# Optimization experiments

Hardware: AMD Instinct MI355X
Metric: run time of the kernel (lower is better)

## Reference

```python
import jax, jax.numpy as jnp
import numpy as np
import math

B, T, C_IN = 4, 2048, 1024
HIDDEN, HEADS = 1024, 8
HEAD_DIM = HIDDEN // HEADS
OUT_DIM = 1024
EPS = 1e-8


def setup_inputs() -> dict:
    key = jax.random.key(0)
    ks = jax.random.split(key, 12)
    s_in = 1.0 / math.sqrt(C_IN)
    s_h = 1.0 / math.sqrt(HIDDEN)
    x = jax.random.normal(ks[0], (B, T, C_IN), dtype=jnp.float32)
    # causal keep-mask (True = keep), broadcast over batch
    attn_mask = jnp.broadcast_to(jnp.tril(jnp.ones((T, T), dtype=bool)), (B, T, T))
    Wu = jax.random.normal(ks[1], (HIDDEN, C_IN), dtype=jnp.float32) * s_in
    bu = jnp.zeros((HIDDEN,), dtype=jnp.float32)
    Wv = jax.random.normal(ks[2], (HIDDEN, C_IN), dtype=jnp.float32) * s_in
    bv = jnp.zeros((HIDDEN,), dtype=jnp.float32)
    Wq = jax.random.normal(ks[3], (HIDDEN, C_IN), dtype=jnp.float32) * s_in
    bq = jnp.zeros((HIDDEN,), dtype=jnp.float32)
    Wk = jax.random.normal(ks[4], (HIDDEN, C_IN), dtype=jnp.float32) * s_in
    bk = jnp.zeros((HIDDEN,), dtype=jnp.float32)
    Wf = jax.random.normal(ks[5], (OUT_DIM, HIDDEN), dtype=jnp.float32) * s_h
    bf = jnp.zeros((OUT_DIM,), dtype=jnp.float32)
    g_norm = jnp.ones((HIDDEN,), dtype=jnp.float32)
    return {"x": x, "attn_mask": attn_mask, "Wu": Wu, "bu": bu, "Wv": Wv,
            "bv": bv, "Wq": Wq, "bq": bq, "Wk": Wk, "bk": bk,
            "Wf": Wf, "bf": bf, "g_norm": g_norm}


def _heads(t):  # (B,T,HIDDEN) -> (B,H,T,D)
    b, s, _ = t.shape
    return t.reshape(b, s, HEADS, HEAD_DIM).transpose(0, 2, 1, 3)


def reference(x, attn_mask, Wu, bu, Wv, bv, Wq, bq, Wk, bk, Wf, bf, g_norm):
    silu = jax.nn.silu
    U = silu(x @ Wu.T + bu)
    V = silu(x @ Wv.T + bv)
    Q = silu(x @ Wq.T + bq)
    K = silu(x @ Wk.T + bk)
    Qh, Kh, Vh = _heads(Q), _heads(K), _heads(V)
    scale = 1.0 / math.sqrt(HEAD_DIM)
    logits = jnp.einsum('bhtd,bhsd->bhts', Qh, Kh) * scale
    A = jnp.maximum(silu(logits), 0.0)
    A = jnp.where(attn_mask[:, None, :, :], A, 0.0)
    denom = A.sum(axis=-1, keepdims=True)
    A = jnp.where(denom > 1e-12, A / (denom + EPS), 0.0)
    AVh = jnp.einsum('bhts,bhsd->bhtd', A, Vh)
    AV = AVh.transpose(0, 2, 1, 3).reshape(x.shape[0], x.shape[1], HIDDEN)
    # RMSNorm (torch nn.RMSNorm default eps = dtype eps)
    rms_eps = jnp.finfo(AV.dtype).eps
    AV_norm = AV * jax.lax.rsqrt(jnp.mean(AV * AV, axis=-1, keepdims=True) + rms_eps) * g_norm
    UV = AV_norm * U
    return UV @ Wf.T + bf
```

## Files before the change

### kernel.cpp

```cpp
#include <hip/hip_runtime.h>
#include <hip/hip_bf16.h>
#include <stdint.h>

#define Tlen  2048
#define M_TOK 8192

typedef __attribute__((ext_vector_type(8))) __bf16 bf16x8;
typedef __attribute__((ext_vector_type(4))) float  f32x4;
typedef unsigned short u16;
typedef unsigned int   u32;
typedef unsigned long long u64;

__device__ __forceinline__ float b2f(u16 u) {
  union { float f; u32 i; } v; v.i = ((u32)u) << 16; return v.f;
}
__device__ __forceinline__ u16 f2b(float f) {
  u32 x = __float_as_uint(f);
  return (u16)((x + 0x7FFFu + ((x >> 16) & 1u)) >> 16);
}
__device__ __forceinline__ u32 f2b2(float lo, float hi) {
  __hip_bfloat162 h = __float22bfloat162_rn(float2{lo, hi});
  return *reinterpret_cast<u32*>(&h);
}
__device__ __forceinline__ bf16x8 ld8(const u16* p) {
  return *reinterpret_cast<const bf16x8*>(p);
}
__device__ __forceinline__ bool probe_bf16(const void* g) {
  return *(const u32*)g == 0x3F803F80u;
}
__device__ __forceinline__ void stage8(u16* dst, const void* src, size_t eidx, bool isbf) {
  if (isbf) {
    *(uint4*)dst = *(const uint4*)((const u16*)src + eidx);
  } else {
    const float* f = (const float*)src + eidx;
    float4 a = *(const float4*)f;
    float4 b = *(const float4*)(f + 4);
    u32 t[4] = { f2b2(a.x, a.y), f2b2(a.z, a.w), f2b2(b.x, b.y), f2b2(b.z, b.w) };
    *(uint4*)dst = *(uint4*)t;
  }
}
__device__ __forceinline__ void gl_lds16(const void* g, void* l) {
  __builtin_amdgcn_global_load_lds(
      (const __attribute__((address_space(1))) u32*)g,
      (__attribute__((address_space(3))) u32*)l, 16, 0, 0);
}
__device__ __forceinline__ int swz128(int r, int c) {
  return r * 128 + ((((c >> 3) ^ (r & 15))) << 3) + (c & 7);
}

__global__ __launch_bounds__(256) void prep1(
    const void* __restrict__ x,
    const void* __restrict__ Wu, const void* __restrict__ Wv,
    const void* __restrict__ Wq, const void* __restrict__ Wk,
    const void* __restrict__ bu, const void* __restrict__ bv,
    const void* __restrict__ bq, const void* __restrict__ bk,
    u16* __restrict__ xb, u16* __restrict__ Wcat, u16* __restrict__ bcat,
    const void* __restrict__ gprobe)
{
  const bool isbf = probe_bf16(gprobe);
  long i = (long)blockIdx.x * 256 + threadIdx.x;
  if (i < 1048576) { stage8(&xb[i * 8], x, (size_t)i * 8, isbf); return; }
  i -= 1048576;
  if (i < 524288) {
    int w = (int)(i >> 17); long e = i & 131071;
    const void* s = (w == 0) ? Wu : (w == 1) ? Wv : (w == 2) ? Wq : Wk;
    stage8(&Wcat[((size_t)w << 20) + e * 8], s, (size_t)e * 8, isbf); return;
  }
  i -= 524288;
  if (i < 512) {
    int w = (int)(i >> 7); int e = (int)(i & 127);
    const void* s = (w == 0) ? bu : (w == 1) ? bv : (w == 2) ? bq : bk;
    stage8(&bcat[w * 1024 + e * 8], s, (size_t)e * 8, isbf);
  }
}

__global__ __launch_bounds__(256) void prep2(
    const void* __restrict__ Wf, const void* __restrict__ bf_,
    u16* __restrict__ Wfb, u16* __restrict__ bfb,
    const void* __restrict__ gprobe)
{
  const bool isbf = probe_bf16(gprobe);
  long i = (long)blockIdx.x * 256 + threadIdx.x;
  if (i < 131072) { stage8(&Wfb[i * 8], Wf, (size_t)i * 8, isbf); return; }
  i -= 131072;
  if (i < 128) stage8(&bfb[i * 8], bf_, (size_t)i * 8, isbf);
}

__global__ __launch_bounds__(256) void gemm_proj(
    const u16* __restrict__ X,
    const u16* __restrict__ W,
    const u16* __restrict__ bias,
    u16* __restrict__ U, u16* __restrict__ Vt,
    u16* __restrict__ Qb, u16* __restrict__ Kb)
{
  __shared__ u16 SMEM[16384];
  u16* Xs = SMEM;
  u16* Ws = SMEM + 8192;
  const int tid  = threadIdx.x;
  const int lane = tid & 63;
  const int wave = tid >> 6;
  const int l15  = lane & 15;
  const int quad = lane >> 4;
  const int wr   = wave & 1;
  const int wc   = wave >> 1;
  const int m0 = blockIdx.y * 128;
  const int n0 = blockIdx.x * 128;

  const int ro = lane >> 3;
  const int ch = lane & 7;
  const int cc = ch ^ ro;

  f32x4 acc[4][4] = {};

  for (int k0 = 0; k0 < 1024; k0 += 64) {
    __syncthreads();
#pragma unroll
    for (int j = 0; j < 4; j++) {
      int r0 = wave * 32 + j * 8;
      gl_lds16(X + (size_t)(m0 + r0 + ro) * 1024 + k0 + cc * 8, &Xs[r0 * 64]);
      gl_lds16(W + (size_t)(n0 + r0 + ro) * 1024 + k0 + cc * 8, &Ws[r0 * 64]);
    }
    __syncthreads();

#pragma unroll
    for (int kk = 0; kk < 64; kk += 32) {
      bf16x8 a[4], b[4];
      const int g = (kk >> 3) + quad;
      const int lch = (g ^ (l15 & 7)) << 3;
#pragma unroll
      for (int mt = 0; mt < 4; mt++)
        a[mt] = ld8(&Xs[(wr * 64 + mt * 16 + l15) * 64 + lch]);
#pragma unroll
      for (int nt = 0; nt < 4; nt++)
        b[nt] = ld8(&Ws[(wc * 64 + nt * 16 + l15) * 64 + lch]);
#pragma unroll
      for (int mt = 0; mt < 4; mt++)
#pragma unroll
        for (int nt = 0; nt < 4; nt++)
          acc[mt][nt] = __builtin_amdgcn_mfma_f32_16x16x32_bf16(a[mt], b[nt], acc[mt][nt], 0, 0, 0);
    }
  }

  const int grp = blockIdx.x >> 3;

  if (grp != 1) {
    u16* dst = (grp == 0) ? U : (grp == 2) ? Qb : Kb;
    const float postmul = (grp == 3) ? 0.08838834764831845f : 1.0f;
#pragma unroll
    for (int nt = 0; nt < 4; nt++) {
      int ng = n0 + wc * 64 + nt * 16 + l15;
      float bv = b2f(bias[ng]);
      int ncol = ng & 1023;
#pragma unroll
      for (int mt = 0; mt < 4; mt++) {
#pragma unroll
        for (int r = 0; r < 4; r++) {
          int m = m0 + wr * 64 + mt * 16 + quad * 4 + r;
          float v = acc[mt][nt][r] + bv;
          v = v * __builtin_amdgcn_rcpf(1.0f + __expf(-v));
          dst[(size_t)m * 1024 + ncol] = f2b(v * postmul);
        }
      }
    }
    return;
  }

  u16* Ls = SMEM;
  __syncthreads();
#pragma unroll
  for (int nt = 0; nt < 4; nt++) {
    int ng = n0 + wc * 64 + nt * 16 + l15;
    float bv = b2f(bias[ng]);
    int nl = wc * 64 + nt * 16 + l15;
#pragma unroll
    for (int mt = 0; mt < 4; mt++) {
      float vv[4];
#pragma unroll
      for (int r = 0; r < 4; r++) {
        float v = acc[mt][nt][r] + bv;
        vv[r] = v * __builtin_amdgcn_rcpf(1.0f + __expf(-v));
      }
      int ml = wr * 64 + mt * 16 + quad * 4;
      u64 pk = (u64)f2b2(vv[0], vv[1]) | ((u64)f2b2(vv[2], vv[3]) << 32);
      *(u64*)&Ls[swz128(nl, ml)] = pk;
    }
  }
  __syncthreads();

  const int rr = tid & 127;
  const int c0 = tid >> 7;
  const int bh = (blockIdx.y >> 4) * 8 + (blockIdx.x & 7);
  const int t0 = (blockIdx.y & 15) * 128;
#pragma unroll
  for (int p = 0; p < 8; p++) {
    int chunk = c0 + p * 2;
    uint4 vv = *(const uint4*)&Ls[swz128(rr, chunk * 8)];
    *(uint4*)&Vt[((size_t)bh * 128 + rr) * 2048 + t0 + chunk * 8] = vv;
  }
}

__global__ __launch_bounds__(256) void gemm_final(
    const u16* __restrict__ X,
    const u16* __restrict__ W,
    const u16* __restrict__ bias,
    float* __restrict__ O)
{
  __shared__ u16 Xs[128 * 64];
  __shared__ u16 Ws[64 * 64];
  const int tid  = threadIdx.x;
  const int lane = tid & 63;
  const int wave = tid >> 6;
  const int l15  = lane & 15;
  const int quad = lane >> 4;
  const int m0 = blockIdx.y * 128;
  const int n0 = blockIdx.x * 64;

  const int ro = lane >> 3;
  const int ch = lane & 7;
  const int cc = ch ^ ro;

  f32x4 acc[2][4] = {};

  for (int k0 = 0; k0 < 1024; k0 += 64) {
    __syncthreads();
#pragma unroll
    for (int j = 0; j < 4; j++) {
      int r0 = wave * 32 + j * 8;
      gl_lds16(X + (size_t)(m0 + r0 + ro) * 1024 + k0 + cc * 8, &Xs[r0 * 64]);
    }
#pragma unroll
    for (int j = 0; j < 2; j++) {
      int r0 = wave * 16 + j * 8;
      gl_lds16(W + (size_t)(n0 + r0 + ro) * 1024 + k0 + cc * 8, &Ws[r0 * 64]);
    }
    __syncthreads();

#pragma unroll
    for (int kk = 0; kk < 64; kk += 32) {
      bf16x8 a[2], b[4];
      const int g = (kk >> 3) + quad;
      const int lch = (g ^ (l15 & 7)) << 3;
#pragma unroll
      for (int mt = 0; mt < 2; mt++)
        a[mt] = ld8(&Xs[(wave * 32 + mt * 16 + l15) * 64 + lch]);
#pragma unroll
      for (int nt = 0; nt < 4; nt++)
        b[nt] = ld8(&Ws[(nt * 16 + l15) * 64 + lch]);
#pragma unroll
      for (int mt = 0; mt < 2; mt++)
#pragma unroll
        for (int nt = 0; nt < 4; nt++)
          acc[mt][nt] = __builtin_amdgcn_mfma_f32_16x16x32_bf16(a[mt], b[nt], acc[mt][nt], 0, 0, 0);
    }
  }

#pragma unroll
  for (int nt = 0; nt < 4; nt++) {
    int n = n0 + nt * 16 + l15;
    float bv = b2f(bias[n]);
#pragma unroll
    for (int mt = 0; mt < 2; mt++)
#pragma unroll
      for (int r = 0; r < 4; r++) {
        int m = m0 + wave * 32 + mt * 16 + quad * 4 + r;
        O[(size_t)m * 1024 + n] = acc[mt][nt][r] + bv;
      }
  }
}

__global__ __launch_bounds__(256, 4) void attn_kernel(
    const u16* __restrict__ Q,
    const u16* __restrict__ K,
    const u16* __restrict__ Vt,
    u16* __restrict__ AV)
{
  __shared__ u16 Ks[64 * 128];
  __shared__ u16 Vts[128 * 64];
  u16* As = Ks;

  const int tid  = threadIdx.x;
  const int lane = tid & 63;
  const int wave = tid >> 6;
  const int l15  = lane & 15;
  const int quad = lane >> 4;
  const int qt = 31 - (blockIdx.x >> 5);
  const int bh = blockIdx.x & 31;
  const int q0 = qt * 64;
  const size_t rowbase = (size_t)(bh >> 3) * Tlen;
  const int cbase = (bh & 7) * 128;
  const size_t vbase = (size_t)bh * 128 * 2048;
  const int mrow = wave * 16;

  bf16x8 bq[4];
#pragma unroll
  for (int kk = 0; kk < 4; kk++)
    bq[kk] = ld8(&Q[(rowbase + q0 + mrow + l15) * 1024 + cbase + kk * 32 + quad * 8]);

  f32x4 avacc[8] = {};
  float denom = 0.f;
  const int t_abs = q0 + mrow + l15;

  for (int s0 = 0; s0 <= q0; s0 += 64) {
    __syncthreads();
    {
      const int ro16 = lane >> 4, ch16 = lane & 15;
#pragma unroll
      for (int j = 0; j < 4; j++) {
        int r0 = wave * 16 + j * 4;
        int cc = ch16 ^ ((r0 + ro16) & 15);
        gl_lds16(&K[(rowbase + s0 + r0 + ro16) * 1024 + cbase + cc * 8], &Ks[r0 * 128]);
      }
      const int ro8 = lane >> 3, ch8 = lane & 7;
#pragma unroll
      for (int j = 0; j < 4; j++) {
        int d0 = wave * 32 + j * 8;
        int cc = ch8 ^ ((d0 + ro8) & 7);
        gl_lds16(&Vt[vbase + (size_t)(d0 + ro8) * 2048 + s0 + cc * 8], &Vts[d0 * 64]);
      }
    }
    __syncthreads();

    f32x4 sacc[4] = {};
#pragma unroll
    for (int kk = 0; kk < 4; kk++) {
      bf16x8 a[4];
      const int lch = (((kk * 4) + quad) ^ l15) << 3;
#pragma unroll
      for (int nt = 0; nt < 4; nt++)
        a[nt] = ld8(&Ks[(nt * 16 + l15) * 128 + lch]);
#pragma unroll
      for (int nt = 0; nt < 4; nt++)
        sacc[nt] = __builtin_amdgcn_mfma_f32_16x16x32_bf16(a[nt], bq[kk], sacc[nt], 0, 0, 0);
    }
    __syncthreads();

    const bool maskneed = (s0 + 63 > q0 + mrow);
    float rs = 0.f;
#pragma unroll
    for (int nt = 0; nt < 4; nt++) {
      float aa[4];
#pragma unroll
      for (int r = 0; r < 4; r++) {
        int s_abs = s0 + nt * 16 + quad * 4 + r;
        float z = sacc[nt][r];
        float a = fmaxf(z, 0.f) * __builtin_amdgcn_rcpf(1.0f + __expf(-z));
        if (maskneed && (s_abs > t_abs)) a = 0.0f;
        rs += a;
        aa[r] = a;
      }
      u64 pk = (u64)f2b2(aa[0], aa[1]) | ((u64)f2b2(aa[2], aa[3]) << 32);
      *(u64*)&As[(mrow + l15) * 72 + nt * 16 + quad * 4] = pk;
    }
    rs += __shfl_xor(rs, 16);
    rs += __shfl_xor(rs, 32);
    denom += rs;

#pragma unroll
    for (int kk = 0; kk < 2; kk++) {
      bf16x8 a, b[8];
      const int lch8 = (((kk * 4) + quad) ^ (l15 & 7)) << 3;
      a = ld8(&As[(mrow + l15) * 72 + kk * 32 + quad * 8]);
#pragma unroll
      for (int dt = 0; dt < 8; dt++)
        b[dt] = ld8(&Vts[(dt * 16 + l15) * 64 + lch8]);
#pragma unroll
      for (int dt = 0; dt < 8; dt++)
        avacc[dt] = __builtin_amdgcn_mfma_f32_16x16x32_bf16(a, b[dt], avacc[dt], 0, 0, 0);
    }
  }

  __syncthreads();
  u16* Ls = Ks;
#pragma unroll
  for (int r = 0; r < 4; r++) {
    float dn = __shfl(denom, (lane & 48) | (quad * 4 + r));
    float sc = (dn > 1e-12f) ? __builtin_amdgcn_rcpf(dn + 1e-8f) : 0.0f;
    int rl = mrow + quad * 4 + r;
#pragma unroll
    for (int dt = 0; dt < 8; dt++)
      Ls[swz128(rl, dt * 16 + l15)] = f2b(avacc[dt][r] * sc);
  }
  __syncthreads();

  const int rr = tid & 63;
  const int c0 = tid >> 6;
#pragma unroll
  for (int p = 0; p < 4; p++) {
    int chunk = c0 + p * 4;
    uint4 vv = *(const uint4*)&Ls[swz128(rr, chunk * 8)];
    *(uint4*)&AV[(rowbase + q0 + rr) * 1024 + cbase + chunk * 8] = vv;
  }
}

__global__ __launch_bounds__(256) void rms_mul(
    const u16* __restrict__ AV, const u16* __restrict__ U,
    const void* __restrict__ g, u16* __restrict__ Y)
{
  const bool isbf = probe_bf16(g);
  const int row = blockIdx.x;
  const int tid = threadIdx.x;
  const size_t base = (size_t)row * 1024;
  uint2 pav = *(const uint2*)&AV[base + tid * 4];
  const u16* pe = (const u16*)&pav;
  float v[4];
  float ss = 0.f;
#pragma unroll
  for (int j = 0; j < 4; j++) { v[j] = b2f(pe[j]); ss += v[j] * v[j]; }
#pragma unroll
  for (int m = 1; m < 64; m <<= 1) ss += __shfl_xor(ss, m);
  __shared__ float red[4];
  if ((tid & 63) == 0) red[tid >> 6] = ss;
  __syncthreads();
  float tot = red[0] + red[1] + red[2] + red[3];
  float rinv = rsqrtf(tot * (1.0f / 1024.0f) + 1.1920929e-7f);
  uint2 pu = *(const uint2*)&U[base + tid * 4];
  const u16* ue = (const u16*)&pu;
  u16 out4[4];
#pragma unroll
  for (int j = 0; j < 4; j++) {
    float gj = isbf ? b2f(((const u16*)g)[tid * 4 + j]) : ((const float*)g)[tid * 4 + j];
    out4[j] = f2b(v[j] * rinv * gj * b2f(ue[j]));
  }
  *(uint2*)&Y[base + tid * 4] = *(uint2*)out4;
}

extern "C" void kernel_launch(void* const* d_in, const int* in_sizes, int n_in,
                              void* d_out, int out_size, void* d_ws, size_t ws_size,
                              hipStream_t stream)
{
  (void)in_sizes; (void)out_size; (void)ws_size;
  const int off = (n_in >= 13) ? 0 : -1;
  const void* x   = d_in[0];
  const void* Wu  = d_in[2 + off];
  const void* bu  = d_in[3 + off];
  const void* Wv  = d_in[4 + off];
  const void* bv  = d_in[5 + off];
  const void* Wq  = d_in[6 + off];
  const void* bq  = d_in[7 + off];
  const void* Wk  = d_in[8 + off];
  const void* bk  = d_in[9 + off];
  const void* Wf  = d_in[10 + off];
  const void* bf_ = d_in[11 + off];
  const void* gn  = d_in[12 + off];

  const size_t NELT = (size_t)M_TOK * 1024;
  u16* xb  = (u16*)d_ws;
  u16* U   = xb + NELT;
  u16* Vt  = U  + NELT;
  u16* Qb  = Vt + NELT;
  u16* Kb  = Qb + NELT;
  u16* AVb = Qb;
  u16* Y   = Kb;
  u16* Wfb = xb;
  u16* bfb = xb + (size_t)1024 * 1024;

  u16* Wcat = (u16*)d_out;
  u16* bcat = Wcat + (size_t)4096 * 1024;

  prep1<<<dim3(6146), 256, 0, stream>>>(x, Wu, Wv, Wq, Wk, bu, bv, bq, bk,
                                        xb, Wcat, bcat, gn);

  gemm_proj<<<dim3(32, 64), 256, 0, stream>>>(xb, Wcat, bcat, U, Vt, Qb, Kb);

  prep2<<<dim3(513), 256, 0, stream>>>(Wf, bf_, Wfb, bfb, gn);

  attn_kernel<<<dim3(1024), 256, 0, stream>>>(Qb, Kb, Vt, AVb);
  rms_mul<<<dim3(M_TOK), 256, 0, stream>>>(AVb, U, gn, Y);

  gemm_final<<<dim3(16, 64), 256, 0, stream>>>(Y, Wfb, bfb, (float*)d_out);
}
```

Measured before the change: 349.8 us.

## Double attention query tile to 128 rows per block for K/V reuse

Each attention block now processes 128 query rows (two 16-row m-tiles per wave) instead of 64, reusing each K/V LDS tile for twice as many queries and halving the grid. The A staging buffer switches from a padded stride to an XOR-swizzled 64-wide layout. This cuts global K/V loads and barrier overhead per query, at the cost of higher register pressure, fewer blocks, and idle waves on diagonal tiles.

```diff
diff --git a/kernel.cpp b/kernel.cpp
--- a/kernel.cpp
+++ b/kernel.cpp
@@ -268,39 +268,41 @@
   }
 }
 
-__global__ __launch_bounds__(256, 4) void attn_kernel(
+__global__ __launch_bounds__(256) void attn_kernel(
     const u16* __restrict__ Q,
     const u16* __restrict__ K,
     const u16* __restrict__ Vt,
     u16* __restrict__ AV)
 {
-  __shared__ u16 Ks[64 * 128];
-  __shared__ u16 Vts[128 * 64];
-  u16* As = Ks;
+  __shared__ u16 SMEM[16384];
+  u16* Ks  = SMEM;
+  u16* Vts = SMEM + 8192;
+  u16* As  = SMEM;
 
   const int tid  = threadIdx.x;
   const int lane = tid & 63;
   const int wave = tid >> 6;
   const int l15  = lane & 15;
   const int quad = lane >> 4;
-  const int qt = 31 - (blockIdx.x >> 5);
+  const int qt = 15 - (blockIdx.x >> 5);
   const int bh = blockIdx.x & 31;
-  const int q0 = qt * 64;
+  const int q0 = qt * 128;
   const size_t rowbase = (size_t)(bh >> 3) * Tlen;
   const int cbase = (bh & 7) * 128;
   const size_t vbase = (size_t)bh * 128 * 2048;
-  const int mrow = wave * 16;
-
-  bf16x8 bq[4];
-#pragma unroll
-  for (int kk = 0; kk < 4; kk++)
-    bq[kk] = ld8(&Q[(rowbase + q0 + mrow + l15) * 1024 + cbase + kk * 32 + quad * 8]);
-
-  f32x4 avacc[8] = {};
-  float denom = 0.f;
-  const int t_abs = q0 + mrow + l15;
-
-  for (int s0 = 0; s0 <= q0; s0 += 64) {
+  const int mrow = wave * 32;
+
+  bf16x8 bq[2][4];
+#pragma unroll
+  for (int mt = 0; mt < 2; mt++)
+#pragma unroll
+    for (int kk = 0; kk < 4; kk++)
+      bq[mt][kk] = ld8(&Q[(rowbase + q0 + mrow + mt * 16 + l15) * 1024 + cbase + kk * 32 + quad * 8]);
+
+  f32x4 avacc[2][8] = {};
+  float denom[2] = {0.f, 0.f};
+
+  for (int s0 = 0; s0 <= q0 + 64; s0 += 64) {
     __syncthreads();
     {
       const int ro16 = lane >> 4, ch16 = lane & 15;
@@ -320,73 +322,93 @@
     }
     __syncthreads();
 
-    f32x4 sacc[4] = {};
-#pragma unroll
-    for (int kk = 0; kk < 4; kk++) {
-      bf16x8 a[4];
-      const int lch = (((kk * 4) + quad) ^ l15) << 3;
-#pragma unroll
-      for (int nt = 0; nt < 4; nt++)
-        a[nt] = ld8(&Ks[(nt * 16 + l15) * 128 + lch]);
-#pragma unroll
-      for (int nt = 0; nt < 4; nt++)
-        sacc[nt] = __builtin_amdgcn_mfma_f32_16x16x32_bf16(a[nt], bq[kk], sacc[nt], 0, 0, 0);
-    }
-    __syncthreads();
-
-    const bool maskneed = (s0 + 63 > q0 + mrow);
-    float rs = 0.f;
-#pragma unroll
-    for (int nt = 0; nt < 4; nt++) {
-      float aa[4];
-#pragma unroll
-      for (int r = 0; r < 4; r++) {
-        int s_abs = s0 + nt * 16 + quad * 4 + r;
-        float z = sacc[nt][r];
-        float a = fmaxf(z, 0.f) * __builtin_amdgcn_rcpf(1.0f + __expf(-z));
-        if (maskneed && (s_abs > t_abs)) a = 0.0f;
-        rs += a;
-        aa[r] = a;
-      }
-      u64 pk = (u64)f2b2(aa[0], aa[1]) | ((u64)f2b2(aa[2], aa[3]) << 32);
-      *(u64*)&As[(mrow + l15) * 72 + nt * 16 + quad * 4] = pk;
-    }
-    rs += __shfl_xor(rs, 16);
-    rs += __shfl_xor(rs, 32);
-    denom += rs;
-
-#pragma unroll
-    for (int kk = 0; kk < 2; kk++) {
-      bf16x8 a, b[8];
-      const int lch8 = (((kk * 4) + quad) ^ (l15 & 7)) << 3;
-      a = ld8(&As[(mrow + l15) * 72 + kk * 32 + quad * 8]);
+    const bool active = (s0 <= q0 + mrow + 31);
+    f32x4 sacc[2][4] = {};
+    if (active) {
+#pragma unroll
+      for (int kk = 0; kk < 4; kk++) {
+        bf16x8 a[4];
+        const int lch = (((kk * 4) + quad) ^ l15) << 3;
+#pragma unroll
+        for (int nt = 0; nt < 4; nt++)
+          a[nt] = ld8(&Ks[(nt * 16 + l15) * 128 + lch]);
+#pragma unroll
+        for (int nt = 0; nt < 4; nt++)
+#pragma unroll
+          for (int mt = 0; mt < 2; mt++)
+            sacc[mt][nt] = __builtin_amdgcn_mfma_f32_16x16x32_bf16(a[nt], bq[mt][kk], sacc[mt][nt], 0, 0, 0);
+      }
+    }
+    __syncthreads();
+
+    if (active) {
+#pragma unroll
+      for (int mt = 0; mt < 2; mt++) {
+        const int t_abs = q0 + mrow + mt * 16 + l15;
+        const bool maskneed = (s0 + 63 > q0 + mrow + mt * 16);
+        float rs = 0.f;
+#pragma unroll
+        for (int nt = 0; nt < 4; nt++) {
+          float aa[4];
+#pragma unroll
+          for (int r = 0; r < 4; r++) {
+            int s_abs = s0 + nt * 16 + quad * 4 + r;
+            float z = sacc[mt][nt][r];
+            float a = fmaxf(z, 0.f) * __builtin_amdgcn_rcpf(1.0f + __expf(-z));
+            if (maskneed && (s_abs > t_abs)) a = 0.0f;
+            rs += a;
+            aa[r] = a;
+          }
+          u64 pk = (u64)f2b2(aa[0], aa[1]) | ((u64)f2b2(aa[2], aa[3]) << 32);
+          int addr = (mrow + mt * 16 + l15) * 64 +
+                     (((nt * 2 + (quad >> 1)) ^ (l15 & 7)) << 3) + (quad & 1) * 4;
+          *(u64*)&As[addr] = pk;
+        }
+        rs += __shfl_xor(rs, 16);
+        rs += __shfl_xor(rs, 32);
+        denom[mt] += rs;
+      }
+
+#pragma unroll
+      for (int kk = 0; kk < 2; kk++) {
+        bf16x8 a[2], b[8];
+        const int lch8 = (((kk * 4) + quad) ^ (l15 & 7)) << 3;
+#pragma unroll
+        for (int mt = 0; mt < 2; mt++)
+          a[mt] = ld8(&As[(mrow + mt * 16 + l15) * 64 + lch8]);
+#pragma unroll
+        for (int dt = 0; dt < 8; dt++)
+          b[dt] = ld8(&Vts[(dt * 16 + l15) * 64 + lch8]);
+#pragma unroll
+        for (int mt = 0; mt < 2; mt++)
+#pragma unroll
+          for (int dt = 0; dt < 8; dt++)
+            avacc[mt][dt] = __builtin_amdgcn_mfma_f32_16x16x32_bf16(a[mt], b[dt], avacc[mt][dt], 0, 0, 0);
+      }
+    }
+  }
+
+  __syncthreads();
+  u16* Ls = SMEM;
+#pragma unroll
+  for (int mt = 0; mt < 2; mt++) {
+#pragma unroll
+    for (int r = 0; r < 4; r++) {
+      float dn = __shfl(denom[mt], (lane & 48) | (quad * 4 + r));
+      float sc = (dn > 1e-12f) ? __builtin_amdgcn_rcpf(dn + 1e-8f) : 0.0f;
+      int rl = mrow + mt * 16 + quad * 4 + r;
 #pragma unroll
       for (int dt = 0; dt < 8; dt++)
-        b[dt] = ld8(&Vts[(dt * 16 + l15) * 64 + lch8]);
-#pragma unroll
-      for (int dt = 0; dt < 8; dt++)
-        avacc[dt] = __builtin_amdgcn_mfma_f32_16x16x32_bf16(a, b[dt], avacc[dt], 0, 0, 0);
-    }
-  }
-
+        Ls[swz128(rl, dt * 16 + l15)] = f2b(avacc[mt][dt][r] * sc);
+    }
+  }
   __syncthreads();
-  u16* Ls = Ks;
-#pragma unroll
-  for (int r = 0; r < 4; r++) {
-    float dn = __shfl(denom, (lane & 48) | (quad * 4 + r));
-    float sc = (dn > 1e-12f) ? __builtin_amdgcn_rcpf(dn + 1e-8f) : 0.0f;
-    int rl = mrow + quad * 4 + r;
-#pragma unroll
-    for (int dt = 0; dt < 8; dt++)
-      Ls[swz128(rl, dt * 16 + l15)] = f2b(avacc[dt][r] * sc);
-  }
-  __syncthreads();
-
-  const int rr = tid & 63;
-  const int c0 = tid >> 6;
-#pragma unroll
-  for (int p = 0; p < 4; p++) {
-    int chunk = c0 + p * 4;
+
+  const int rr = tid & 127;
+  const int c0 = tid >> 7;
+#pragma unroll
+  for (int p = 0; p < 8; p++) {
+    int chunk = c0 + p * 2;
     uint4 vv = *(const uint4*)&Ls[swz128(rr, chunk * 8)];
     *(uint4*)&AV[(rowbase + q0 + rr) * 1024 + cbase + chunk * 8] = vv;
   }
@@ -464,7 +486,7 @@
 
   prep2<<<dim3(513), 256, 0, stream>>>(Wf, bf_, Wfb, bfb, gn);
 
-  attn_kernel<<<dim3(1024), 256, 0, stream>>>(Qb, Kb, Vt, AVb);
+  attn_kernel<<<dim3(512), 256, 0, stream>>>(Qb, Kb, Vt, AVb);
   rms_mul<<<dim3(M_TOK), 256, 0, stream>>>(AVb, U, gn, Y);
 
   gemm_final<<<dim3(16, 64), 256, 0, stream>>>(Y, Wfb, bfb, (float*)d_out);
```

Result: slower. 390.9 us (+11.7%).
